# Performance work log

Measured on AMD Instinct MI355X. Metric: run time of the kernel, lower is better.

The kernel has to match this reference:

```python
import jax, jax.numpy as jnp
import numpy as np

B, S, D = 2, 2048, 1024
H = 16
DH = D // H  # 64


def setup_inputs() -> dict:
    key = jax.random.key(0)
    ks = jax.random.split(key, 7)
    q = jax.random.normal(ks[0], (B, S, D), dtype=jnp.float32)
    k = jax.random.normal(ks[1], (B, S, D), dtype=jnp.float32)
    v = jax.random.normal(ks[2], (B, S, D), dtype=jnp.float32)
    # torch.rand -> uniform[0,1)
    w_q = jax.random.uniform(ks[3], (D, D), dtype=jnp.float32)
    w_k = jax.random.uniform(ks[4], (DH, D), dtype=jnp.float32)
    w_v = jax.random.uniform(ks[5], (DH, D), dtype=jnp.float32)
    w_out = jax.random.uniform(ks[6], (D, D), dtype=jnp.float32)
    return {"q": q, "k": k, "v": v, "w_q": w_q, "w_k": w_k, "w_v": w_v, "w_out": w_out}


def reference(q, k, v, w_q, w_k, w_v, w_out):
    # F.linear(x, W) = x @ W.T
    qp = jnp.einsum('bsd,ed->bse', q, w_q)          # [B,S,D]
    kp = jnp.einsum('bsd,hd->bsh', k, w_k)          # [B,S,DH] shared K head
    vp = jnp.einsum('bsd,hd->bsh', v, w_v)          # [B,S,DH] shared V head
    qh = qp.reshape(B, S, H, DH).transpose(0, 2, 1, 3)  # [B,H,S,DH]
    scale = 1.0 / jnp.sqrt(jnp.float32(DH))
    scores = jnp.einsum('bhsd,btd->bhst', qh, kp) * scale  # [B,H,S,S]
    attn = jax.nn.softmax(scores, axis=-1)
    out = jnp.einsum('bhst,btd->bhsd', attn, vp)    # [B,H,S,DH]
    out = out.transpose(0, 2, 1, 3).reshape(B, S, D)
    return jnp.einsum('bsd,ed->bse', out, w_out)
```

## Files before the change

kernel.cpp:

```cpp
#include <hip/hip_runtime.h>
#include <hip/hip_bf16.h>
#include <stdint.h>


#define B_   2
#define S_   2048
#define D_   1024
#define H_   16
#define DH_  64
#define MTOT (B_ * S_)
#define NSPL 4

typedef short bf16x8 __attribute__((ext_vector_type(8)));
typedef float f32x4 __attribute__((ext_vector_type(4)));
typedef float f32x16 __attribute__((ext_vector_type(16)));
typedef short short4v __attribute__((ext_vector_type(4)));
typedef unsigned uint4v __attribute__((ext_vector_type(4)));

__device__ __forceinline__ short f2bf(float f) {
  unsigned u = __float_as_uint(f);
  u += 0x7FFF + ((u >> 16) & 1);
  return (short)(u >> 16);
}
__device__ __forceinline__ float bf2f(short h) {
  return __uint_as_float(((unsigned)(unsigned short)h) << 16);
}
struct bfpair { short hi, lo; };
__device__ __forceinline__ bfpair split2(float x) {
  bfpair p;
  p.hi = f2bf(x);
  p.lo = f2bf(x - bf2f(p.hi));
  return p;
}
__device__ __forceinline__ unsigned cvtpk(float lo, float hi) {
  unsigned r;
  asm("v_cvt_pk_bf16_f32 %0, %1, %2" : "=v"(r) : "v"(lo), "v"(hi));
  return r;
}

__device__ __forceinline__ void glds16(const void* g, void* l) {
  __builtin_amdgcn_global_load_lds((const __attribute__((address_space(1))) void*)g,
                                   (__attribute__((address_space(3))) void*)l, 16, 0, 0);
}

__global__ __launch_bounds__(256) void cvt_split(
    const float* __restrict__ q, const float* __restrict__ k, const float* __restrict__ v,
    const float* __restrict__ wq, const float* __restrict__ wk, const float* __restrict__ wv,
    const float* __restrict__ wo,
    short* qhi, short* qlo, short* khi, short* klo, short* vb,
    short* wqh, short* wql, short* wkh, short* wkl, short* wvb, short* wob) {
  const int U0 = 1048576, U1 = 2097152, U2 = 3145728, U3 = 3407872,
            U4 = 3424256, U5 = 3440640, U6 = 3702784;
  for (int u = blockIdx.x * blockDim.x + threadIdx.x; u < U6; u += gridDim.x * blockDim.x) {
    const float* s; short* dh; short* dl; int r;
    if (u < U0)      { s = q;  dh = qhi; dl = qlo; r = u; }
    else if (u < U1) { s = k;  dh = khi; dl = klo; r = u - U0; }
    else if (u < U2) { s = v;  dh = vb;  dl = nullptr; r = u - U1; }
    else if (u < U3) { s = wq; dh = wqh; dl = wql; r = u - U2; }
    else if (u < U4) { s = wk; dh = wkh; dl = wkl; r = u - U3; }
    else if (u < U5) { s = wv; dh = wvb; dl = nullptr; r = u - U4; }
    else             { s = wo; dh = wob; dl = nullptr; r = u - U5; }
    float4 x = *(const float4*)(s + (size_t)r * 4);
    bfpair p0 = split2(x.x), p1 = split2(x.y), p2 = split2(x.z), p3 = split2(x.w);
    short4v yh, yl;
    yh.x = p0.hi; yh.y = p1.hi; yh.z = p2.hi; yh.w = p3.hi;
    yl.x = p0.lo; yl.y = p1.lo; yl.z = p2.lo; yl.w = p3.lo;
    *(short4v*)(dh + (size_t)r * 4) = yh;
    if (dl) *(short4v*)(dl + (size_t)r * 4) = yl;
  }
}

template <int NPROD, int MODE>
__global__ __launch_bounds__(256) void gemm3(
    const short* __restrict__ Ah, const short* __restrict__ Al,
    const short* __restrict__ Bh, const short* __restrict__ Bl,
    short* __restrict__ Ch, short* __restrict__ Cl, float* __restrict__ Cf,
    int K, int lda, int ldb, int ldc, float alpha) {
  __shared__ alignas(16) short Ash[4096], Asl[4096], Bsh[4096], Bsl[4096];
  const int tid = threadIdx.x;
  const int lane = tid & 63, w = tid >> 6;
  const int c = lane & 15, g = lane >> 4;
  const int wm = w >> 1, wn = w & 1;
  const int bm = blockIdx.x * 64, bn = blockIdx.y * 64;
  const int sr = lane >> 3;
  const int scs = ((lane & 7) ^ sr) * 8;

  f32x4 acc[2][2] = {};
  for (int k0 = 0; k0 < K; k0 += 64) {
    glds16(Ah + (size_t)(bm + w * 8 + sr) * lda + k0 + scs,      Ash + w * 512);
    glds16(Ah + (size_t)(bm + 32 + w * 8 + sr) * lda + k0 + scs, Ash + 2048 + w * 512);
    glds16(Bh + (size_t)(bn + w * 8 + sr) * ldb + k0 + scs,      Bsh + w * 512);
    glds16(Bh + (size_t)(bn + 32 + w * 8 + sr) * ldb + k0 + scs, Bsh + 2048 + w * 512);
    if constexpr (NPROD == 3) {
      glds16(Al + (size_t)(bm + w * 8 + sr) * lda + k0 + scs,      Asl + w * 512);
      glds16(Al + (size_t)(bm + 32 + w * 8 + sr) * lda + k0 + scs, Asl + 2048 + w * 512);
      glds16(Bl + (size_t)(bn + w * 8 + sr) * ldb + k0 + scs,      Bsl + w * 512);
      glds16(Bl + (size_t)(bn + 32 + w * 8 + sr) * ldb + k0 + scs, Bsl + 2048 + w * 512);
    }
    __syncthreads();
#pragma unroll
    for (int kk = 0; kk < 2; ++kk) {
      bf16x8 ah[2], bh[2], al[2], bl[2];
#pragma unroll
      for (int mt = 0; mt < 2; ++mt) {
        int row = wm * 32 + mt * 16 + c;
        int so = row * 64 + (((kk * 4 + g) ^ (row & 7)) * 8);
        ah[mt] = *(const bf16x8*)(Ash + so);
        if constexpr (NPROD == 3) al[mt] = *(const bf16x8*)(Asl + so);
      }
#pragma unroll
      for (int nt = 0; nt < 2; ++nt) {
        int row = wn * 32 + nt * 16 + c;
        int so = row * 64 + (((kk * 4 + g) ^ (row & 7)) * 8);
        bh[nt] = *(const bf16x8*)(Bsh + so);
        if constexpr (NPROD == 3) bl[nt] = *(const bf16x8*)(Bsl + so);
      }
#pragma unroll
      for (int mt = 0; mt < 2; ++mt)
#pragma unroll
        for (int nt = 0; nt < 2; ++nt) {
          acc[mt][nt] = __builtin_amdgcn_mfma_f32_16x16x32_bf16(ah[mt], bh[nt], acc[mt][nt], 0, 0, 0);
          if constexpr (NPROD == 3) {
            acc[mt][nt] = __builtin_amdgcn_mfma_f32_16x16x32_bf16(ah[mt], bl[nt], acc[mt][nt], 0, 0, 0);
            acc[mt][nt] = __builtin_amdgcn_mfma_f32_16x16x32_bf16(al[mt], bh[nt], acc[mt][nt], 0, 0, 0);
          }
        }
    }
    __syncthreads();
  }
#pragma unroll
  for (int mt = 0; mt < 2; ++mt) {
#pragma unroll
    for (int nt = 0; nt < 2; ++nt) {
#pragma unroll
      for (int r = 0; r < 4; ++r) {
        int m = bm + wm * 32 + mt * 16 + g * 4 + r;
        int n = bn + wn * 32 + nt * 16 + c;
        float val = acc[mt][nt][r] * alpha;
        if constexpr (MODE == 0) {
          bfpair pr = split2(val);
          Ch[(size_t)m * ldc + n] = pr.hi;
          Cl[(size_t)m * ldc + n] = pr.lo;
        } else if constexpr (MODE == 3) {
          Cf[(size_t)m * ldc + n] = val;
        } else if constexpr (MODE == 4) {
          size_t off = (((size_t)(m >> 5) * 4 + (n >> 4)) * 64 +
                        ((m & 31) + 32 * ((n >> 3) & 1))) * 8 + (n & 7);
          bfpair pr = split2(val);
          Ch[off] = pr.hi;
          Cl[off] = pr.lo;
        } else {
          size_t off = ((((size_t)(m >> 5) * 2 + (n >> 5)) * 2 + ((m >> 4) & 1)) * 64 +
                        ((n & 31) + 32 * ((m >> 3) & 1))) * 8 + (m & 7);
          Ch[off] = f2bf(val);
        }
      }
    }
  }
}

__global__ __launch_bounds__(256) void mqa_attn(
    const short* __restrict__ qph, const short* __restrict__ qpl,
    const short* __restrict__ pkh, const short* __restrict__ pkl,
    const short* __restrict__ pv, short* __restrict__ pO, float* __restrict__ pML) {
  const int tid = threadIdx.x;
  const int lane = tid & 63, w = tid >> 6;
  const int j = lane & 31, b5 = lane >> 5;
  const int qt = blockIdx.x, h = blockIdx.y;
  const int b = blockIdx.z >> 2, sp = blockIdx.z & 3;
  const int q0 = qt * 128 + w * 32;
  const int kvbeg = sp * (S_ / NSPL), kvend = kvbeg + S_ / NSPL;

  const size_t qbase = (size_t)(b * S_ + q0 + j) * D_ + h * DH_ + b5 * 8;
  bf16x8 qh[4], ql[4];
#pragma unroll
  for (int m = 0; m < 4; ++m) {
    qh[m] = *(const bf16x8*)(qph + qbase + m * 16);
    ql[m] = *(const bf16x8*)(qpl + qbase + m * 16);
  }

  float mrow = -1.0e30f, lrow = 0.f;
  f32x16 o0 = {}, o1 = {};

  for (int kv0 = kvbeg; kv0 < kvend; kv0 += 32) {
    const size_t tg = (size_t)((b * S_ + kv0) >> 5);
    const short* kb = pkh + tg * 2048 + lane * 8;
    const short* kb2 = pkl + tg * 2048 + lane * 8;
    bf16x8 kh[4], kl[4];
#pragma unroll
    for (int m = 0; m < 4; ++m) {
      kh[m] = *(const bf16x8*)(kb + m * 512);
      kl[m] = *(const bf16x8*)(kb2 + m * 512);
    }
    f32x16 s = {};
#pragma unroll
    for (int m = 0; m < 4; ++m)
      s = __builtin_amdgcn_mfma_f32_32x32x16_bf16(kh[m], qh[m], s, 0, 0, 0);
#pragma unroll
    for (int m = 0; m < 4; ++m)
      s = __builtin_amdgcn_mfma_f32_32x32x16_bf16(kl[m], qh[m], s, 0, 0, 0);
#pragma unroll
    for (int m = 0; m < 4; ++m)
      s = __builtin_amdgcn_mfma_f32_32x32x16_bf16(kh[m], ql[m], s, 0, 0, 0);
    float mx = s[0];
#pragma unroll
    for (int r = 1; r < 16; ++r) mx = fmaxf(mx, s[r]);
    mx = fmaxf(mx, __shfl_xor(mx, 32));
    if (!__all(mx - mrow <= 8.0f)) {
      float mn = fmaxf(mrow, mx);
      float scale = exp2f(mrow - mn);
      mrow = mn;
      lrow *= scale;
      o0 *= scale;
      o1 *= scale;
    }
    float p[16];
#pragma unroll
    for (int r = 0; r < 16; ++r) p[r] = exp2f(s[r] - mrow);
    float rs = (((p[0] + p[1]) + (p[2] + p[3])) + ((p[4] + p[5]) + (p[6] + p[7]))) +
               (((p[8] + p[9]) + (p[10] + p[11])) + ((p[12] + p[13]) + (p[14] + p[15])));
    rs += __shfl_xor(rs, 32);
    lrow += rs;
    auto r0 = __builtin_amdgcn_permlane32_swap(cvtpk(p[0], p[1]),   cvtpk(p[4], p[5]),   false, false);
    auto r1 = __builtin_amdgcn_permlane32_swap(cvtpk(p[2], p[3]),   cvtpk(p[6], p[7]),   false, false);
    auto r2 = __builtin_amdgcn_permlane32_swap(cvtpk(p[8], p[9]),   cvtpk(p[12], p[13]), false, false);
    auto r3 = __builtin_amdgcn_permlane32_swap(cvtpk(p[10], p[11]), cvtpk(p[14], p[15]), false, false);
    union { uint4v u; bf16x8 v; } pa0, pa1;
    pa0.u = (uint4v){r0[0], r1[0], r0[1], r1[1]};
    pa1.u = (uint4v){r2[0], r3[0], r2[1], r3[1]};
    const short* vbp = pv + tg * 2048 + lane * 8;
    bf16x8 va00 = *(const bf16x8*)(vbp);
    bf16x8 va01 = *(const bf16x8*)(vbp + 512);
    bf16x8 va10 = *(const bf16x8*)(vbp + 1024);
    bf16x8 va11 = *(const bf16x8*)(vbp + 1536);
    o0 = __builtin_amdgcn_mfma_f32_32x32x16_bf16(va00, pa0.v, o0, 0, 0, 0);
    o0 = __builtin_amdgcn_mfma_f32_32x32x16_bf16(va01, pa1.v, o0, 0, 0, 0);
    o1 = __builtin_amdgcn_mfma_f32_32x32x16_bf16(va10, pa0.v, o1, 0, 0, 0);
    o1 = __builtin_amdgcn_mfma_f32_32x32x16_bf16(va11, pa1.v, o1, 0, 0, 0);
  }
  const size_t tok = (size_t)(b * S_ + q0 + j);
  const size_t obase = ((size_t)sp * MTOT + tok) * D_ + h * DH_;
#pragma unroll
  for (int r = 0; r < 16; ++r) {
    int dh0 = (r & 3) + 8 * (r >> 2) + 4 * b5;
    pO[obase + dh0] = f2bf(o0[r]);
    pO[obase + 32 + dh0] = f2bf(o1[r]);
  }
  if (b5 == 0) {
    size_t mb = (((size_t)sp * MTOT + tok) * H_ + h) * 2;
    pML[mb] = mrow;
    pML[mb + 1] = lrow;
  }
}

__global__ __launch_bounds__(256) void attn_merge(
    const short* __restrict__ pO, const float* __restrict__ pML,
    short* __restrict__ ao) {
  int qd = blockIdx.x * 256 + threadIdx.x;
  size_t idx = (size_t)qd * 4;
  int tok = (int)(idx >> 10);
  int h = (int)((idx >> 6) & 15);
  float ms[NSPL], ls[NSPL], mm = -1.0e30f;
#pragma unroll
  for (int s = 0; s < NSPL; ++s) {
    size_t mb = (((size_t)s * MTOT + tok) * H_ + h) * 2;
    ms[s] = pML[mb];
    ls[s] = pML[mb + 1];
    mm = fmaxf(mm, ms[s]);
  }
  float num[4] = {}, den = 0.f;
#pragma unroll
  for (int s = 0; s < NSPL; ++s) {
    float e = exp2f(ms[s] - mm);
    den += ls[s] * e;
    short4v o4 = *(const short4v*)(pO + (size_t)s * MTOT * D_ + idx);
    num[0] += bf2f(o4.x) * e;
    num[1] += bf2f(o4.y) * e;
    num[2] += bf2f(o4.z) * e;
    num[3] += bf2f(o4.w) * e;
  }
  float inv = 1.0f / den;
  short4v y;
  y.x = f2bf(num[0] * inv);
  y.y = f2bf(num[1] * inv);
  y.z = f2bf(num[2] * inv);
  y.w = f2bf(num[3] * inv);
  *(short4v*)(ao + idx) = y;
}

extern "C" void kernel_launch(void* const* d_in, const int* in_sizes, int n_in,
                              void* d_out, int out_size, void* d_ws, size_t ws_size,
                              hipStream_t stream) {
  const float* q  = (const float*)d_in[0];
  const float* k  = (const float*)d_in[1];
  const float* v  = (const float*)d_in[2];
  const float* wq = (const float*)d_in[3];
  const float* wk = (const float*)d_in[4];
  const float* wv = (const float*)d_in[5];
  const float* wo = (const float*)d_in[6];

  short* p = (short*)d_ws;
  short* qhi = p; p += 4194304;
  short* qlo = p; p += 4194304;
  short* khi = p; p += 4194304;
  short* klo = p; p += 4194304;
  short* vb  = p; p += 4194304;
  short* wqh = p; p += 1048576;
  short* wql = p; p += 1048576;
  short* wkh = p; p += 65536;
  short* wkl = p; p += 65536;
  short* wvb = p; p += 65536;
  short* wob = p; p += 1048576;
  short* qph = p; p += 4194304;
  short* qpl = p; p += 4194304;
  short* pkh = p; p += 524288;
  short* pkl = p; p += 524288;
  short* pv  = p; p += 524288;
  short* pO  = qhi;
  float* pML = (float*)vb;
  short* ao  = qph;

  cvt_split<<<dim3(2048), dim3(256), 0, stream>>>(q, k, v, wq, wk, wv, wo,
      qhi, qlo, khi, klo, vb, wqh, wql, wkh, wkl, wvb, wob);
  gemm3<3, 0><<<dim3(64, 16), dim3(256), 0, stream>>>(qhi, qlo, wqh, wql, qph, qpl,
      nullptr, 1024, 1024, 1024, 1024, 0.125f * 1.44269504f);
  gemm3<3, 4><<<dim3(64, 1), dim3(256), 0, stream>>>(khi, klo, wkh, wkl, pkh, pkl,
      nullptr, 1024, 1024, 1024, 64, 1.0f);
  gemm3<1, 5><<<dim3(64, 1), dim3(256), 0, stream>>>(vb, nullptr, wvb, nullptr, pv,
      nullptr, nullptr, 1024, 1024, 1024, 64, 1.0f);
  mqa_attn<<<dim3(S_ / 128, 16, B_ * NSPL), dim3(256), 0, stream>>>(
      qph, qpl, pkh, pkl, pv, pO, pML);
  attn_merge<<<dim3(MTOT * D_ / 4 / 256), dim3(256), 0, stream>>>(pO, pML, ao);
  gemm3<1, 3><<<dim3(64, 16), dim3(256), 0, stream>>>(ao, nullptr, wob, nullptr,
      nullptr, nullptr, (float*)d_out, 1024, 1024, 1024, 1024, 1.0f);
}
```

Before: 203.1 us.

## Double-buffer shared K/V tiles in LDS via async global-to-LDS loads

After: 243.0 us. 1.2x slower.

```diff
diff --git a/kernel.cpp b/kernel.cpp
--- a/kernel.cpp
+++ b/kernel.cpp
@@ -36,6 +36,11 @@
   unsigned r;
   asm("v_cvt_pk_bf16_f32 %0, %1, %2" : "=v"(r) : "v"(lo), "v"(hi));
   return r;
+}
+__device__ __forceinline__ float2 xhalf(float x) {
+  unsigned u = __float_as_uint(x);
+  auto sw = __builtin_amdgcn_permlane32_swap(u, u, false, false);
+  return make_float2(__uint_as_float(sw[0]), __uint_as_float(sw[1]));
 }
 
 __device__ __forceinline__ void glds16(const void* g, void* l) {
@@ -163,6 +168,7 @@
     const short* __restrict__ qph, const short* __restrict__ qpl,
     const short* __restrict__ pkh, const short* __restrict__ pkl,
     const short* __restrict__ pv, short* __restrict__ pO, float* __restrict__ pML) {
+  __shared__ alignas(16) short Kls[2][3][2048];
   const int tid = threadIdx.x;
   const int lane = tid & 63, w = tid >> 6;
   const int j = lane & 31, b5 = lane >> 5;
@@ -179,18 +185,31 @@
     ql[m] = *(const bf16x8*)(qpl + qbase + m * 16);
   }
 
+  auto stage = [&](int buf, size_t tg) {
+#pragma unroll
+    for (int i = 0; i < 3; ++i) {
+      int cc = w + 4 * i;
+      int part = cc >> 2, qq = cc & 3;
+      const short* src = (part == 0 ? pkh : (part == 1 ? pkl : pv));
+      glds16(src + tg * 2048 + qq * 512 + lane * 8, &Kls[buf][part][qq * 512]);
+    }
+  };
+
   float mrow = -1.0e30f, lrow = 0.f;
   f32x16 o0 = {}, o1 = {};
 
+  const size_t tg0 = (size_t)((b * S_ + kvbeg) >> 5);
+  stage(0, tg0);
+  __syncthreads();
+  int cur = 0;
+
   for (int kv0 = kvbeg; kv0 < kvend; kv0 += 32) {
-    const size_t tg = (size_t)((b * S_ + kv0) >> 5);
-    const short* kb = pkh + tg * 2048 + lane * 8;
-    const short* kb2 = pkl + tg * 2048 + lane * 8;
+    if (kv0 + 32 < kvend) stage(cur ^ 1, tg0 + ((kv0 - kvbeg) >> 5) + 1);
     bf16x8 kh[4], kl[4];
 #pragma unroll
     for (int m = 0; m < 4; ++m) {
-      kh[m] = *(const bf16x8*)(kb + m * 512);
-      kl[m] = *(const bf16x8*)(kb2 + m * 512);
+      kh[m] = *(const bf16x8*)(&Kls[cur][0][m * 512 + lane * 8]);
+      kl[m] = *(const bf16x8*)(&Kls[cur][1][m * 512 + lane * 8]);
     }
     f32x16 s = {};
 #pragma unroll
@@ -202,10 +221,14 @@
 #pragma unroll
     for (int m = 0; m < 4; ++m)
       s = __builtin_amdgcn_mfma_f32_32x32x16_bf16(kh[m], ql[m], s, 0, 0, 0);
-    float mx = s[0];
-#pragma unroll
-    for (int r = 1; r < 16; ++r) mx = fmaxf(mx, s[r]);
-    mx = fmaxf(mx, __shfl_xor(mx, 32));
+    float a0 = fmaxf(s[0], s[1]), a1 = fmaxf(s[2], s[3]),
+          a2 = fmaxf(s[4], s[5]), a3 = fmaxf(s[6], s[7]),
+          a4 = fmaxf(s[8], s[9]), a5 = fmaxf(s[10], s[11]),
+          a6 = fmaxf(s[12], s[13]), a7 = fmaxf(s[14], s[15]);
+    float b0 = fmaxf(a0, a1), b1 = fmaxf(a2, a3), b2 = fmaxf(a4, a5), b3 = fmaxf(a6, a7);
+    float mx = fmaxf(fmaxf(b0, b1), fmaxf(b2, b3));
+    float2 xh = xhalf(mx);
+    mx = fmaxf(xh.x, xh.y);
     if (!__all(mx - mrow <= 8.0f)) {
       float mn = fmaxf(mrow, mx);
       float scale = exp2f(mrow - mn);
@@ -219,7 +242,8 @@
     for (int r = 0; r < 16; ++r) p[r] = exp2f(s[r] - mrow);
     float rs = (((p[0] + p[1]) + (p[2] + p[3])) + ((p[4] + p[5]) + (p[6] + p[7]))) +
                (((p[8] + p[9]) + (p[10] + p[11])) + ((p[12] + p[13]) + (p[14] + p[15])));
-    rs += __shfl_xor(rs, 32);
+    float2 rh = xhalf(rs);
+    rs = rh.x + rh.y;
     lrow += rs;
     auto r0 = __builtin_amdgcn_permlane32_swap(cvtpk(p[0], p[1]),   cvtpk(p[4], p[5]),   false, false);
     auto r1 = __builtin_amdgcn_permlane32_swap(cvtpk(p[2], p[3]),   cvtpk(p[6], p[7]),   false, false);
@@ -228,15 +252,16 @@
     union { uint4v u; bf16x8 v; } pa0, pa1;
     pa0.u = (uint4v){r0[0], r1[0], r0[1], r1[1]};
     pa1.u = (uint4v){r2[0], r3[0], r2[1], r3[1]};
-    const short* vbp = pv + tg * 2048 + lane * 8;
-    bf16x8 va00 = *(const bf16x8*)(vbp);
-    bf16x8 va01 = *(const bf16x8*)(vbp + 512);
-    bf16x8 va10 = *(const bf16x8*)(vbp + 1024);
-    bf16x8 va11 = *(const bf16x8*)(vbp + 1536);
+    bf16x8 va00 = *(const bf16x8*)(&Kls[cur][2][lane * 8]);
+    bf16x8 va01 = *(const bf16x8*)(&Kls[cur][2][512 + lane * 8]);
+    bf16x8 va10 = *(const bf16x8*)(&Kls[cur][2][1024 + lane * 8]);
+    bf16x8 va11 = *(const bf16x8*)(&Kls[cur][2][1536 + lane * 8]);
     o0 = __builtin_amdgcn_mfma_f32_32x32x16_bf16(va00, pa0.v, o0, 0, 0, 0);
     o0 = __builtin_amdgcn_mfma_f32_32x32x16_bf16(va01, pa1.v, o0, 0, 0, 0);
     o1 = __builtin_amdgcn_mfma_f32_32x32x16_bf16(va10, pa0.v, o1, 0, 0, 0);
     o1 = __builtin_amdgcn_mfma_f32_32x32x16_bf16(va11, pa1.v, o1, 0, 0, 0);
+    __syncthreads();
+    cur ^= 1;
   }
   const size_t tok = (size_t)(b * S_ + q0 + j);
   const size_t obase = ((size_t)sp * MTOT + tok) * D_ + h * DH_;
```

## Use 128x128-tile GEMM for Q and output projections; swap shuffles for permlane

Applied to the files above, without the earlier changes.

Result: slower. 217.2 us (+6.9%).

```diff
diff --git a/kernel.cpp b/kernel.cpp
--- a/kernel.cpp
+++ b/kernel.cpp
@@ -36,6 +36,11 @@
   unsigned r;
   asm("v_cvt_pk_bf16_f32 %0, %1, %2" : "=v"(r) : "v"(lo), "v"(hi));
   return r;
+}
+__device__ __forceinline__ float2 xhalf(float x) {
+  unsigned u = __float_as_uint(x);
+  auto sw = __builtin_amdgcn_permlane32_swap(u, u, false, false);
+  return make_float2(__uint_as_float(sw[0]), __uint_as_float(sw[1]));
 }
 
 __device__ __forceinline__ void glds16(const void* g, void* l) {
@@ -137,13 +142,7 @@
         int m = bm + wm * 32 + mt * 16 + g * 4 + r;
         int n = bn + wn * 32 + nt * 16 + c;
         float val = acc[mt][nt][r] * alpha;
-        if constexpr (MODE == 0) {
-          bfpair pr = split2(val);
-          Ch[(size_t)m * ldc + n] = pr.hi;
-          Cl[(size_t)m * ldc + n] = pr.lo;
-        } else if constexpr (MODE == 3) {
-          Cf[(size_t)m * ldc + n] = val;
-        } else if constexpr (MODE == 4) {
+        if constexpr (MODE == 4) {
           size_t off = (((size_t)(m >> 5) * 4 + (n >> 4)) * 64 +
                         ((m & 31) + 32 * ((n >> 3) & 1))) * 8 + (n & 7);
           bfpair pr = split2(val);
@@ -153,6 +152,89 @@
           size_t off = ((((size_t)(m >> 5) * 2 + (n >> 5)) * 2 + ((m >> 4) & 1)) * 64 +
                         ((n & 31) + 32 * ((m >> 3) & 1))) * 8 + (m & 7);
           Ch[off] = f2bf(val);
+        }
+      }
+    }
+  }
+}
+
+template <int NPROD, int MODE>
+__global__ __launch_bounds__(256) void gemm128(
+    const short* __restrict__ Ah, const short* __restrict__ Al,
+    const short* __restrict__ Bh, const short* __restrict__ Bl,
+    short* __restrict__ Ch, short* __restrict__ Cl, float* __restrict__ Cf,
+    int K, int lda, int ldb, int ldc, float alpha) {
+  constexpr bool SPLIT = (NPROD == 3);
+  __shared__ alignas(16) short Ash[8192];
+  __shared__ alignas(16) short Bsh[8192];
+  __shared__ alignas(16) short Asl[SPLIT ? 8192 : 16];
+  __shared__ alignas(16) short Bsl[SPLIT ? 8192 : 16];
+  const int tid = threadIdx.x;
+  const int lane = tid & 63, w = tid >> 6;
+  const int c = lane & 15, g = lane >> 4;
+  const int wm = w >> 1, wn = w & 1;
+  const int bm = blockIdx.x * 128, bn = blockIdx.y * 128;
+  const int sr = lane >> 3;
+  const int scs = ((lane & 7) ^ sr) * 8;
+
+  f32x4 acc[4][4] = {};
+  for (int k0 = 0; k0 < K; k0 += 64) {
+#pragma unroll
+    for (int i = 0; i < 4; ++i) {
+      int rowb = i * 32 + w * 8;
+      glds16(Ah + (size_t)(bm + rowb + sr) * lda + k0 + scs, Ash + rowb * 64);
+      glds16(Bh + (size_t)(bn + rowb + sr) * ldb + k0 + scs, Bsh + rowb * 64);
+      if constexpr (SPLIT) {
+        glds16(Al + (size_t)(bm + rowb + sr) * lda + k0 + scs, Asl + rowb * 64);
+        glds16(Bl + (size_t)(bn + rowb + sr) * ldb + k0 + scs, Bsl + rowb * 64);
+      }
+    }
+    __syncthreads();
+#pragma unroll
+    for (int kk = 0; kk < 2; ++kk) {
+      bf16x8 ah[4], bh[4], al[4], bl[4];
+#pragma unroll
+      for (int mt = 0; mt < 4; ++mt) {
+        int row = wm * 64 + mt * 16 + c;
+        int so = row * 64 + (((kk * 4 + g) ^ (row & 7)) * 8);
+        ah[mt] = *(const bf16x8*)(Ash + so);
+        if constexpr (SPLIT) al[mt] = *(const bf16x8*)(Asl + so);
+      }
+#pragma unroll
+      for (int nt = 0; nt < 4; ++nt) {
+        int row = wn * 64 + nt * 16 + c;
+        int so = row * 64 + (((kk * 4 + g) ^ (row & 7)) * 8);
+        bh[nt] = *(const bf16x8*)(Bsh + so);
+        if constexpr (SPLIT) bl[nt] = *(const bf16x8*)(Bsl + so);
+      }
+#pragma unroll
+      for (int mt = 0; mt < 4; ++mt)
+#pragma unroll
+        for (int nt = 0; nt < 4; ++nt) {
+          acc[mt][nt] = __builtin_amdgcn_mfma_f32_16x16x32_bf16(ah[mt], bh[nt], acc[mt][nt], 0, 0, 0);
+          if constexpr (SPLIT) {
+            acc[mt][nt] = __builtin_amdgcn_mfma_f32_16x16x32_bf16(ah[mt], bl[nt], acc[mt][nt], 0, 0, 0);
+            acc[mt][nt] = __builtin_amdgcn_mfma_f32_16x16x32_bf16(al[mt], bh[nt], acc[mt][nt], 0, 0, 0);
+          }
+        }
+    }
+    __syncthreads();
+  }
+#pragma unroll
+  for (int mt = 0; mt < 4; ++mt) {
+#pragma unroll
+    for (int nt = 0; nt < 4; ++nt) {
+#pragma unroll
+      for (int r = 0; r < 4; ++r) {
+        int m = bm + wm * 64 + mt * 16 + g * 4 + r;
+        int n = bn + wn * 64 + nt * 16 + c;
+        float val = acc[mt][nt][r] * alpha;
+        if constexpr (MODE == 0) {
+          bfpair pr = split2(val);
+          Ch[(size_t)m * ldc + n] = pr.hi;
+          Cl[(size_t)m * ldc + n] = pr.lo;
+        } else {
+          Cf[(size_t)m * ldc + n] = val;
         }
       }
     }
@@ -202,10 +284,14 @@
 #pragma unroll
     for (int m = 0; m < 4; ++m)
       s = __builtin_amdgcn_mfma_f32_32x32x16_bf16(kh[m], ql[m], s, 0, 0, 0);
-    float mx = s[0];
-#pragma unroll
-    for (int r = 1; r < 16; ++r) mx = fmaxf(mx, s[r]);
-    mx = fmaxf(mx, __shfl_xor(mx, 32));
+    float a0 = fmaxf(s[0], s[1]), a1 = fmaxf(s[2], s[3]),
+          a2 = fmaxf(s[4], s[5]), a3 = fmaxf(s[6], s[7]),
+          a4 = fmaxf(s[8], s[9]), a5 = fmaxf(s[10], s[11]),
+          a6 = fmaxf(s[12], s[13]), a7 = fmaxf(s[14], s[15]);
+    float b0 = fmaxf(a0, a1), b1 = fmaxf(a2, a3), b2 = fmaxf(a4, a5), b3 = fmaxf(a6, a7);
+    float mx = fmaxf(fmaxf(b0, b1), fmaxf(b2, b3));
+    float2 xh = xhalf(mx);
+    mx = fmaxf(xh.x, xh.y);
     if (!__all(mx - mrow <= 8.0f)) {
       float mn = fmaxf(mrow, mx);
       float scale = exp2f(mrow - mn);
@@ -219,7 +305,8 @@
     for (int r = 0; r < 16; ++r) p[r] = exp2f(s[r] - mrow);
     float rs = (((p[0] + p[1]) + (p[2] + p[3])) + ((p[4] + p[5]) + (p[6] + p[7]))) +
                (((p[8] + p[9]) + (p[10] + p[11])) + ((p[12] + p[13]) + (p[14] + p[15])));
-    rs += __shfl_xor(rs, 32);
+    float2 rh = xhalf(rs);
+    rs = rh.x + rh.y;
     lrow += rs;
     auto r0 = __builtin_amdgcn_permlane32_swap(cvtpk(p[0], p[1]),   cvtpk(p[4], p[5]),   false, false);
     auto r1 = __builtin_amdgcn_permlane32_swap(cvtpk(p[2], p[3]),   cvtpk(p[6], p[7]),   false, false);
@@ -322,7 +409,7 @@
 
   cvt_split<<<dim3(2048), dim3(256), 0, stream>>>(q, k, v, wq, wk, wv, wo,
       qhi, qlo, khi, klo, vb, wqh, wql, wkh, wkl, wvb, wob);
-  gemm3<3, 0><<<dim3(64, 16), dim3(256), 0, stream>>>(qhi, qlo, wqh, wql, qph, qpl,
+  gemm128<3, 0><<<dim3(32, 8), dim3(256), 0, stream>>>(qhi, qlo, wqh, wql, qph, qpl,
       nullptr, 1024, 1024, 1024, 1024, 0.125f * 1.44269504f);
   gemm3<3, 4><<<dim3(64, 1), dim3(256), 0, stream>>>(khi, klo, wkh, wkl, pkh, pkl,
       nullptr, 1024, 1024, 1024, 64, 1.0f);
@@ -331,6 +418,6 @@
   mqa_attn<<<dim3(S_ / 128, 16, B_ * NSPL), dim3(256), 0, stream>>>(
       qph, qpl, pkh, pkl, pv, pO, pML);
   attn_merge<<<dim3(MTOT * D_ / 4 / 256), dim3(256), 0, stream>>>(pO, pML, ao);
-  gemm3<1, 3><<<dim3(64, 16), dim3(256), 0, stream>>>(ao, nullptr, wob, nullptr,
+  gemm128<1, 3><<<dim3(32, 8), dim3(256), 0, stream>>>(ao, nullptr, wob, nullptr,
       nullptr, nullptr, (float*)d_out, 1024, 1024, 1024, 1024, 1.0f);
 }
```
